# Performance work log

Hardware: AMD Instinct MI355X
Metric: run time of the kernel (lower is better)

The kernel has to match this reference:

```python
import jax, jax.numpy as jnp
import numpy as np

SIZE = 65536
MAX_EDGES = 16777216  # n_edges = min(0.1*SIZE^2, MAX_EDGES) = MAX_EDGES, so all edges active


def setup_inputs() -> dict:
    key = jax.random.key(0)
    k1, k2, k3, k4 = jax.random.split(key, 4)
    x = jax.random.normal(k1, (SIZE,), dtype=jnp.float32)
    edge_weights = jax.random.normal(k2, (MAX_EDGES,), dtype=jnp.float32) * (2.0 / SIZE) ** 0.5
    bias = jnp.zeros((SIZE,), dtype=jnp.float32)
    src = jax.random.randint(k3, (MAX_EDGES,), 0, SIZE, dtype=jnp.int64 if jax.config.jax_enable_x64 else jnp.int32)
    dst = jax.random.randint(k4, (MAX_EDGES,), 0, SIZE, dtype=jnp.int64 if jax.config.jax_enable_x64 else jnp.int32)
    return {"x": x, "edge_weights": edge_weights, "bias": bias, "src": src, "dst": dst}


def reference(x, edge_weights, bias, src, dst):
    # gather -> elementwise multiply -> scatter_add -> + bias
    weighted = x[src] * edge_weights                    # [E]
    out = jax.ops.segment_sum(weighted, dst, num_segments=SIZE)  # [size]
    return out + bias
```

## Files before the change

kernel.cpp:

```cpp
#include <hip/hip_runtime.h>


#define NNODES  65536
#define NEDGES  16777216
#define RANGES  2
#define BINS    (NNODES / RANGES)
#define THREADS 1024
#define NCOPIES 128
#define GROUPS  16
#define CPG     (NCOPIES / GROUPS)

__global__ __launch_bounds__(THREADS, 4) void hist_kernel(
    const float* __restrict__ x,
    const float* __restrict__ w,
    const int*   __restrict__ src,
    const int*   __restrict__ dst,
    float*       __restrict__ ws,
    int B)
{
    extern __shared__ float h[];

    const int b  = blockIdx.x;
    const int r  = b & (RANGES - 1);
    const int c  = b >> 1;
    const int lo = r * BINS;

    for (int i = threadIdx.x; i < BINS; i += THREADS) h[i] = 0.0f;
    __syncthreads();

    const int4*   src4 = (const int4*)src;
    const int4*   dst4 = (const int4*)dst;
    const float4* wgt4 = (const float4*)w;

    const int n8 = NEDGES / 8;
    for (int g = c * THREADS + (int)threadIdx.x; g < n8; g += B * THREADS) {
        int4   sa = src4[2 * g], sb = src4[2 * g + 1];
        int4   da = dst4[2 * g], db = dst4[2 * g + 1];
        float4 wa = wgt4[2 * g], wb = wgt4[2 * g + 1];

        int      s[8]  = { sa.x, sa.y, sa.z, sa.w, sb.x, sb.y, sb.z, sb.w };
        unsigned bin[8] = {
            (unsigned)(da.x - lo), (unsigned)(da.y - lo),
            (unsigned)(da.z - lo), (unsigned)(da.w - lo),
            (unsigned)(db.x - lo), (unsigned)(db.y - lo),
            (unsigned)(db.z - lo), (unsigned)(db.w - lo) };
        float    wv[8] = { wa.x, wa.y, wa.z, wa.w, wb.x, wb.y, wb.z, wb.w };

        float xv[8];
        #pragma unroll
        for (int k = 0; k < 8; ++k) {
            xv[k] = 0.0f;
            if (bin[k] < (unsigned)BINS) xv[k] = x[s[k]];
        }

        __builtin_amdgcn_sched_barrier(0);

        #pragma unroll
        for (int k = 0; k < 8; ++k) {
            if (bin[k] < (unsigned)BINS) atomicAdd(&h[bin[k]], xv[k] * wv[k]);
        }
    }
    __syncthreads();

    float4* outc4 = (float4*)(ws + (size_t)c * NNODES + lo);
    const float4* h4 = (const float4*)h;
    for (int i = threadIdx.x; i < BINS / 4; i += THREADS) outc4[i] = h4[i];
}

__global__ __launch_bounds__(256) void reduceA_kernel(float* __restrict__ ws)
{
    const int NB = NNODES / (256 * 4);
    int g  = blockIdx.x / NB;
    int jb = blockIdx.x % NB;
    int i4 = jb * 256 + (int)threadIdx.x;

    float4* w4 = (float4*)ws;
    const int stride4 = NNODES / 4;

    float4 acc = w4[(size_t)(g * CPG) * stride4 + i4];
    #pragma unroll
    for (int cc = 1; cc < CPG; ++cc) {
        float4 t = w4[(size_t)(g * CPG + cc) * stride4 + i4];
        acc.x += t.x; acc.y += t.y; acc.z += t.z; acc.w += t.w;
    }
    w4[(size_t)(g * CPG) * stride4 + i4] = acc;
}

__global__ __launch_bounds__(256) void reduceB_kernel(
    const float* __restrict__ ws,
    const float* __restrict__ bias,
    float*       __restrict__ out)
{
    int i4 = blockIdx.x * 256 + (int)threadIdx.x;
    const float4* w4 = (const float4*)ws;
    const int stride4 = NNODES / 4;

    float4 acc = ((const float4*)bias)[i4];
    #pragma unroll
    for (int g = 0; g < GROUPS; ++g) {
        float4 t = w4[(size_t)(g * CPG) * stride4 + i4];
        acc.x += t.x; acc.y += t.y; acc.z += t.z; acc.w += t.w;
    }
    ((float4*)out)[i4] = acc;
}

__global__ __launch_bounds__(256) void reduce_generic_kernel(
    const float* __restrict__ ws,
    const float* __restrict__ bias,
    float*       __restrict__ out,
    int B)
{
    int i = blockIdx.x * 256 + (int)threadIdx.x;
    float acc = bias[i];
    for (int cc = 0; cc < B; ++cc) acc += ws[(size_t)cc * NNODES + i];
    out[i] = acc;
}

__global__ __launch_bounds__(256) void init_out_kernel(
    const float* __restrict__ bias, float* __restrict__ out)
{
    int i = blockIdx.x * blockDim.x + threadIdx.x;
    if (i < NNODES) out[i] = bias[i];
}

__global__ __launch_bounds__(256) void edge_atomic_kernel(
    const float* __restrict__ x, const float* __restrict__ w,
    const int* __restrict__ src, const int* __restrict__ dst,
    float* __restrict__ out)
{
    const int n4 = NEDGES / 4;
    int tid = blockIdx.x * blockDim.x + threadIdx.x;
    int stride = gridDim.x * blockDim.x;
    for (int i = tid; i < n4; i += stride) {
        int4 s = ((const int4*)src)[i];
        int4 d = ((const int4*)dst)[i];
        float4 ww = ((const float4*)w)[i];
        atomicAdd(&out[d.x], x[s.x] * ww.x);
        atomicAdd(&out[d.y], x[s.y] * ww.y);
        atomicAdd(&out[d.z], x[s.z] * ww.z);
        atomicAdd(&out[d.w], x[s.w] * ww.w);
    }
}

extern "C" void kernel_launch(void* const* d_in, const int* in_sizes, int n_in,
                              void* d_out, int out_size, void* d_ws, size_t ws_size,
                              hipStream_t stream) {
    const float* x    = (const float*)d_in[0];
    const float* w    = (const float*)d_in[1];
    const float* bias = (const float*)d_in[2];
    const int*   src  = (const int*)d_in[3];
    const int*   dst  = (const int*)d_in[4];
    float* out = (float*)d_out;
    float* ws  = (float*)d_ws;

    size_t copies = ws_size / ((size_t)NNODES * sizeof(float));
    int B = (int)(copies < NCOPIES ? copies : NCOPIES);

    if (B >= 1) {
        hist_kernel<<<B * RANGES, THREADS, BINS * sizeof(float), stream>>>(
            x, w, src, dst, ws, B);
        if (B == NCOPIES) {
            reduceA_kernel<<<GROUPS * (NNODES / 1024), 256, 0, stream>>>(ws);
            reduceB_kernel<<<NNODES / 1024, 256, 0, stream>>>(ws, bias, out);
        } else {
            reduce_generic_kernel<<<NNODES / 256, 256, 0, stream>>>(ws, bias, out, B);
        }
    } else {
        init_out_kernel<<<NNODES / 256, 256, 0, stream>>>(bias, out);
        edge_atomic_kernel<<<4096, 256, 0, stream>>>(x, w, src, dst, out);
    }
}
```

Before: 275.0 us.

## Split gather and scatter into separate kernels with materialized edge products

Adds a two-phase path: a gather kernel computes x[src]*w for every edge into a workspace buffer, then a scatter kernel reads dst and the precomputed products to do shared-memory histogram atomics per range. In the old fused kernel each of the two range blocks re-gathered x for its edges; now the gather happens once and the scatter loop carries no random global loads. The cost is writing and rereading 64MB of products plus needing a larger workspace. The fallback hist_kernel also drops its sched_barrier and the separate load loop.

```diff
diff --git a/kernel.cpp b/kernel.cpp
--- a/kernel.cpp
+++ b/kernel.cpp
@@ -9,6 +9,77 @@
 #define NCOPIES 128
 #define GROUPS  16
 #define CPG     (NCOPIES / GROUPS)
+#define GBLOCKS 256
+
+__global__ __launch_bounds__(THREADS) void gather_kernel(
+    const float* __restrict__ x,
+    const float* __restrict__ w,
+    const int*   __restrict__ src,
+    float*       __restrict__ v)
+{
+    const int4*   src4 = (const int4*)src;
+    const float4* wgt4 = (const float4*)w;
+    float4*       v4   = (float4*)v;
+
+    const int n8     = NEDGES / 8;
+    const int stride = GBLOCKS * THREADS;
+
+    for (int g = blockIdx.x * THREADS + (int)threadIdx.x; g < n8; g += stride) {
+        int4   sa = src4[2 * g], sb = src4[2 * g + 1];
+        float4 wa = wgt4[2 * g], wb = wgt4[2 * g + 1];
+
+        float x0 = x[sa.x], x1 = x[sa.y], x2 = x[sa.z], x3 = x[sa.w];
+        float x4_ = x[sb.x], x5 = x[sb.y], x6 = x[sb.z], x7 = x[sb.w];
+
+        float4 va = { x0 * wa.x, x1 * wa.y, x2 * wa.z, x3 * wa.w };
+        float4 vb = { x4_ * wb.x, x5 * wb.y, x6 * wb.z, x7 * wb.w };
+        v4[2 * g]     = va;
+        v4[2 * g + 1] = vb;
+    }
+}
+
+__global__ __launch_bounds__(THREADS, 4) void scatter_kernel(
+    const int*   __restrict__ dst,
+    const float* __restrict__ v,
+    float*       __restrict__ ws,
+    int B)
+{
+    extern __shared__ float h[];
+
+    const int b  = blockIdx.x;
+    const int r  = b & (RANGES - 1);
+    const int c  = b >> 1;
+    const int lo = r * BINS;
+
+    for (int i = threadIdx.x; i < BINS; i += THREADS) h[i] = 0.0f;
+    __syncthreads();
+
+    const int4*   dst4 = (const int4*)dst;
+    const float4* val4 = (const float4*)v;
+
+    const int n8 = NEDGES / 8;
+    for (int g = c * THREADS + (int)threadIdx.x; g < n8; g += B * THREADS) {
+        int4   da = dst4[2 * g], db = dst4[2 * g + 1];
+        float4 va = val4[2 * g], vb = val4[2 * g + 1];
+
+        unsigned bin[8] = {
+            (unsigned)(da.x - lo), (unsigned)(da.y - lo),
+            (unsigned)(da.z - lo), (unsigned)(da.w - lo),
+            (unsigned)(db.x - lo), (unsigned)(db.y - lo),
+            (unsigned)(db.z - lo), (unsigned)(db.w - lo) };
+        float vv[8] = { va.x, va.y, va.z, va.w, vb.x, vb.y, vb.z, vb.w };
+
+        #pragma unroll
+        for (int k = 0; k < 8; ++k) {
+            if (bin[k] < (unsigned)BINS) atomicAdd(&h[bin[k]], vv[k]);
+        }
+    }
+    __syncthreads();
+
+    float4* outc4 = (float4*)(ws + (size_t)c * NNODES + lo);
+    const float4* h4 = (const float4*)h;
+    for (int i = threadIdx.x; i < BINS / 4; i += THREADS) outc4[i] = h4[i];
+}
 
 __global__ __launch_bounds__(THREADS, 4) void hist_kernel(
     const float* __restrict__ x,
@@ -46,18 +117,9 @@
             (unsigned)(db.z - lo), (unsigned)(db.w - lo) };
         float    wv[8] = { wa.x, wa.y, wa.z, wa.w, wb.x, wb.y, wb.z, wb.w };
 
-        float xv[8];
         #pragma unroll
         for (int k = 0; k < 8; ++k) {
-            xv[k] = 0.0f;
-            if (bin[k] < (unsigned)BINS) xv[k] = x[s[k]];
-        }
-
-        __builtin_amdgcn_sched_barrier(0);
-
-        #pragma unroll
-        for (int k = 0; k < 8; ++k) {
-            if (bin[k] < (unsigned)BINS) atomicAdd(&h[bin[k]], xv[k] * wv[k]);
+            if (bin[k] < (unsigned)BINS) atomicAdd(&h[bin[k]], x[s[k]] * wv[k]);
         }
     }
     __syncthreads();
@@ -151,10 +213,24 @@
     const int*   src  = (const int*)d_in[3];
     const int*   dst  = (const int*)d_in[4];
     float* out = (float*)d_out;
-    float* ws  = (float*)d_ws;
-
-    size_t copies = ws_size / ((size_t)NNODES * sizeof(float));
-    int B = (int)(copies < NCOPIES ? copies : NCOPIES);
+
+    const size_t need_two_phase =
+        ((size_t)NEDGES + (size_t)NCOPIES * NNODES) * sizeof(float);
+
+    if (ws_size >= need_two_phase) {
+        float* v      = (float*)d_ws;
+        float* copies = v + NEDGES;
+        gather_kernel<<<GBLOCKS, THREADS, 0, stream>>>(x, w, src, v);
+        scatter_kernel<<<NCOPIES * RANGES, THREADS, BINS * sizeof(float), stream>>>(
+            dst, v, copies, NCOPIES);
+        reduceA_kernel<<<GROUPS * (NNODES / 1024), 256, 0, stream>>>(copies);
+        reduceB_kernel<<<NNODES / 1024, 256, 0, stream>>>(copies, bias, out);
+        return;
+    }
+
+    float* ws = (float*)d_ws;
+    size_t copies_fit = ws_size / ((size_t)NNODES * sizeof(float));
+    int B = (int)(copies_fit < NCOPIES ? copies_fit : NCOPIES);
 
     if (B >= 1) {
         hist_kernel<<<B * RANGES, THREADS, BINS * sizeof(float), stream>>>(
```

New measurement: 331.9 us. 20.7% more time.
